# Kernel tuning notes

Hardware: AMD Instinct MI355X
Metric: run time of the kernel (lower is better)

## Reference

```python
import jax, jax.numpy as jnp
import numpy as np

NUM_EMBEDDINGS = 1024
EMBEDDING_DIM = 128
COMMITMENT_COST = 1.0
DECAY = 0.99
EPSILON = 1e-05
N_TOKENS = 65536


def setup_inputs() -> dict:
    key = jax.random.key(0)
    k1, k2, k3 = jax.random.split(key, 3)
    inputs = jax.random.normal(k1, (N_TOKENS, EMBEDDING_DIM), dtype=jnp.float32)
    embedding = jax.random.normal(k2, (NUM_EMBEDDINGS, EMBEDDING_DIM), dtype=jnp.float32) * 0.01
    cluster_size = jnp.ones((NUM_EMBEDDINGS,), dtype=jnp.float32)
    embed_avg = jax.random.normal(k3, (NUM_EMBEDDINGS, EMBEDDING_DIM), dtype=jnp.float32) * 0.01
    return {"inputs": inputs, "embedding": embedding,
            "cluster_size": cluster_size, "embed_avg": embed_avg}


def reference(inputs, embedding, cluster_size, embed_avg):
    # inputs: [N, D], embedding: [K, D]
    flat = inputs.reshape(-1, EMBEDDING_DIM)
    distances = (jnp.sum(flat * flat, axis=1, keepdims=True)
                 + jnp.sum(embedding * embedding, axis=1)
                 - 2.0 * flat @ embedding.T)
    idx = jnp.argmin(distances, axis=1)                       # [N]
    quantized = embedding[idx].reshape(inputs.shape)          # direct gather (same math as one-hot matmul)

    # EMA update (training path); one-hot matmuls replaced by bincount/segment_sum
    dw = jnp.zeros((NUM_EMBEDDINGS,), dtype=flat.dtype).at[idx].add(1.0)   # encodings.sum(0)
    new_cluster_size = cluster_size * DECAY + (1.0 - DECAY) * dw
    dw_embed = jax.ops.segment_sum(flat, idx, num_segments=NUM_EMBEDDINGS)  # encodings.T @ flat
    new_embed_avg = embed_avg * DECAY + (1.0 - DECAY) * dw_embed
    n = jnp.sum(new_cluster_size)
    cs = (new_cluster_size + EPSILON) / (n + NUM_EMBEDDINGS * EPSILON) * n
    new_embedding = new_embed_avg / cs[:, None]

    # losses (quantized/inputs detach semantics are identical values in fwd)
    diff2 = jnp.mean((quantized - inputs) ** 2)
    loss = diff2 + COMMITMENT_COST * diff2

    # straight-through estimator: value equals quantized
    quantized_st = inputs + jax.lax.stop_gradient(quantized - inputs)
    return (quantized_st, loss, idx, new_embedding, new_cluster_size, new_embed_avg)
```

## Files before the change

### kernel.cpp

```cpp
#include <hip/hip_runtime.h>

typedef __attribute__((ext_vector_type(8))) _Float16 half8;
typedef __attribute__((ext_vector_type(4))) float f32x4;

constexpr int NTOK = 65536;
constexpr int DIM  = 128;
constexpr int NK   = 1024;

__global__ void bprep_k(const float* __restrict__ emb, char* __restrict__ bp,
                        float* __restrict__ embT, float* __restrict__ e2s,
                        double* __restrict__ en2d, int* __restrict__ nflag) {
  int i = blockIdx.x * 256 + threadIdx.x;
  if (i == 0) *nflag = 0;
  int c = i >> 4;
  int g = i & 15;
  float4 v0 = *(const float4*)&emb[c * 128 + g * 8];
  float4 v1 = *(const float4*)&emb[c * 128 + g * 8 + 4];
  float vf[8] = {v0.x, v0.y, v0.z, v0.w, v1.x, v1.y, v1.z, v1.w};
  half8 hv;
  double pacc = 0.0;
#pragma unroll
  for (int j = 0; j < 8; j++) {
    hv[j] = (_Float16)vf[j];
    embT[(g * 8 + j) * NK + c] = vf[j];
    pacc = fma((double)vf[j], (double)vf[j], pacc);
  }
  int chunk = c >> 5, n = (c >> 4) & 1, cl = c & 15;
  int kk = g >> 2, lo4 = g & 3;
  *(half8*)(bp + chunk * 8192 + kk * 2048 + n * 1024 + (lo4 * 16 + cl) * 16) = hv;
#pragma unroll
  for (int mask = 1; mask < 16; mask <<= 1) pacc += __shfl_xor(pacc, mask);
  if (g == 0) {
    en2d[c] = pacc;
    e2s[c] = (float)(pacc * 134217728.0 + 1073741824.0);
  }
}

__global__ __launch_bounds__(128, 2)
void argmin_k(const float* __restrict__ x, const char* __restrict__ bp,
              const float* __restrict__ e2s, int* __restrict__ idx_arr,
              float* __restrict__ out_idx, int* __restrict__ nflag,
              int* __restrict__ flags) {
  __shared__ unsigned kvs[2][32], k2s[2][32];
  const int t    = threadIdx.x;
  const int lane = t & 63;
  const int w    = t >> 6;
  const int l15  = lane & 15;
  const int lo4  = lane >> 4;
  const int rbase = blockIdx.x * 32;
  const int cbase = w * 16;
  const int lb16 = lane * 16;

  half8 FA[4][2], FB[4][2];

#define LOADG(DST, C, KK)                                                      \
  {                                                                            \
    const char* _b = bp + ((C) * 8192 + (KK) * 2048) + lb16;                   \
    DST[0] = *(const half8*)_b;                                                \
    DST[1] = *(const half8*)(_b + 1024);                                       \
  }

#pragma unroll
  for (int kk = 0; kk < 4; kk++) LOADG(FA[kk], cbase, kk)
#pragma unroll
  for (int kk = 0; kk < 4; kk++) LOADG(FB[kk], cbase + 1, kk)

  half8 ah[2][4];
#pragma unroll
  for (int m = 0; m < 2; m++)
#pragma unroll
    for (int kk = 0; kk < 4; kk++) {
      const float* xp = &x[(rbase + m * 16 + l15) * 128 + kk * 32 + lo4 * 8];
      float4 v0 = *(const float4*)xp;
      float4 v1 = *(const float4*)(xp + 4);
      float vf[8] = {v0.x, v0.y, v0.z, v0.w, v1.x, v1.y, v1.z, v1.w};
      half8 av;
#pragma unroll
      for (int j = 0; j < 8; j++) av[j] = (_Float16)vf[j];
      ah[m][kk] = av;
    }

  unsigned bv[2][4], b2[2][4];
#pragma unroll
  for (int m = 0; m < 2; m++)
#pragma unroll
    for (int r = 0; r < 4; r++) { bv[m][r] = 0xFFFFFFFFu; b2[m][r] = 0xFFFFFFFFu; }

#define MFMA_PHASE(BANK, KK)                                                   \
  {                                                                            \
    acc[0][0] = __builtin_amdgcn_mfma_f32_16x16x32_f16(ah[0][KK], BANK[KK][0], acc[0][0], 0, 0, 0); \
    acc[1][0] = __builtin_amdgcn_mfma_f32_16x16x32_f16(ah[1][KK], BANK[KK][0], acc[1][0], 0, 0, 0); \
    acc[0][1] = __builtin_amdgcn_mfma_f32_16x16x32_f16(ah[0][KK], BANK[KK][1], acc[0][1], 0, 0, 0); \
    acc[1][1] = __builtin_amdgcn_mfma_f32_16x16x32_f16(ah[1][KK], BANK[KK][1], acc[1][1], 0, 0, 0); \
  }

#define KEY_EPI(C)                                                             \
  {                                                                            \
    _Pragma("unroll")                                                          \
    for (int n = 0; n < 2; n++) {                                              \
      unsigned col = (unsigned)((C) * 32 + n * 16 + l15);                      \
      float e2v = n ? e2b : e2a;                                               \
      _Pragma("unroll")                                                        \
      for (int m = 0; m < 2; m++)                                              \
        _Pragma("unroll")                                                      \
        for (int r = 0; r < 4; r++) {                                          \
          float ks = fmaf(acc[m][n][r], -268435456.0f, e2v);                   \
          unsigned key = ((unsigned)ks & 0xFFFFFC00u) | col;                   \
          unsigned old = bv[m][r];                                             \
          bv[m][r] = min(old, key);                                            \
          b2[m][r] = min(b2[m][r], max(old, key));                             \
        }                                                                      \
    }                                                                          \
  }

  for (int i = 0; i < 16; i += 2) {
    const int cg = cbase + i;
    {
      float e2a = e2s[cg * 32 + l15];
      float e2b = e2s[cg * 32 + 16 + l15];
      f32x4 acc[2][2];
#pragma unroll
      for (int m = 0; m < 2; m++)
#pragma unroll
        for (int n = 0; n < 2; n++) acc[m][n] = (f32x4)(0.0f);
#pragma unroll
      for (int kk = 0; kk < 4; kk++) {
        MFMA_PHASE(FA, kk)
        if (i + 2 < 16) LOADG(FA[kk], cg + 2, kk)
      }
      KEY_EPI(cg)
    }
    {
      float e2a = e2s[(cg + 1) * 32 + l15];
      float e2b = e2s[(cg + 1) * 32 + 16 + l15];
      f32x4 acc[2][2];
#pragma unroll
      for (int m = 0; m < 2; m++)
#pragma unroll
        for (int n = 0; n < 2; n++) acc[m][n] = (f32x4)(0.0f);
#pragma unroll
      for (int kk = 0; kk < 4; kk++) {
        MFMA_PHASE(FB, kk)
        if (i + 3 < 16) LOADG(FB[kk], cg + 3, kk)
      }
      KEY_EPI(cg + 1)
    }
  }
#undef LOADG
#undef MFMA_PHASE
#undef KEY_EPI

#pragma unroll
  for (int m = 0; m < 2; m++)
#pragma unroll
    for (int r = 0; r < 4; r++) {
      unsigned v = bv[m][r], v2 = b2[m][r];
      for (int mask = 1; mask < 16; mask <<= 1) {
        unsigned ov = __shfl_xor(v, mask);
        unsigned o2 = __shfl_xor(v2, mask);
        v2 = min(min(v2, o2), max(v, ov));
        v  = min(v, ov);
      }
      if (l15 == 0) {
        int lr = m * 16 + lo4 * 4 + r;
        kvs[w][lr] = v;
        k2s[w][lr] = v2;
      }
    }
  __syncthreads();

  if (t < 32) {
    unsigned va = kvs[0][t], vb = kvs[1][t];
    unsigned v2 = min(min(k2s[0][t], k2s[1][t]), max(va, vb));
    unsigned v  = min(va, vb);
    int row = rbase + t;
    int ii = (int)(v & 1023u);
    idx_arr[row] = ii;
    out_idx[row] = (float)ii;
    if ((v2 >> 10) - (v >> 10) < 79u) {
      int p = atomicAdd(nflag, 1); flags[p] = row;
    }
  }
}

__global__ __launch_bounds__(256)
void fb_k(const float* __restrict__ x, const float* __restrict__ embT,
          const double* __restrict__ en2d, const int* __restrict__ nflag,
          const int* __restrict__ flags, int* __restrict__ idx_arr,
          float* __restrict__ out_idx) {
  int n = *nflag;
  __shared__ double xsh[4][DIM];
  __shared__ double sv[256];
  __shared__ int    si[256];
  int t = threadIdx.x;
  double n0 = en2d[t * 4 + 0], n1 = en2d[t * 4 + 1];
  double n2 = en2d[t * 4 + 2], n3 = en2d[t * 4 + 3];
  for (int base = blockIdx.x * 4; base < n; base += gridDim.x * 4) {
    int nb = min(4, n - base);
    __syncthreads();
    for (int u = t; u < nb * DIM; u += 256) {
      int j = u >> 7, d = u & 127;
      xsh[j][d] = (double)x[flags[base + j] * DIM + d];
    }
    __syncthreads();
    double xe[4][4];
#pragma unroll
    for (int j = 0; j < 4; j++)
#pragma unroll
      for (int q = 0; q < 4; q++) xe[j][q] = 0.0;
    for (int d = 0; d < DIM; d++) {
      float4 v = *(const float4*)&embT[d * NK + t * 4];
      double e0 = (double)v.x, e1 = (double)v.y, e2 = (double)v.z, e3 = (double)v.w;
#pragma unroll
      for (int j = 0; j < 4; j++) {
        double xd = xsh[j][d];
        xe[j][0] = fma(e0, xd, xe[j][0]);
        xe[j][1] = fma(e1, xd, xe[j][1]);
        xe[j][2] = fma(e2, xd, xe[j][2]);
        xe[j][3] = fma(e3, xd, xe[j][3]);
      }
    }
#pragma unroll
    for (int j = 0; j < 4; j++) {
      double s0 = n0 - 2.0 * xe[j][0];
      double s1 = n1 - 2.0 * xe[j][1];
      double s2 = n2 - 2.0 * xe[j][2];
      double s3 = n3 - 2.0 * xe[j][3];
      double bvv = s0; int bii = t * 4;
      if (s1 < bvv) { bvv = s1; bii = t * 4 + 1; }
      if (s2 < bvv) { bvv = s2; bii = t * 4 + 2; }
      if (s3 < bvv) { bvv = s3; bii = t * 4 + 3; }
      sv[t] = bvv; si[t] = bii;
      __syncthreads();
      for (int sh = 128; sh > 0; sh >>= 1) {
        if (t < sh) {
          double ov = sv[t + sh]; int oi = si[t + sh];
          if (ov < sv[t] || (ov == sv[t] && oi < si[t])) { sv[t] = ov; si[t] = oi; }
        }
        __syncthreads();
      }
      if (t == 0 && j < nb) {
        int row = flags[base + j];
        idx_arr[row] = si[0];
        out_idx[row] = (float)si[0];
      }
      __syncthreads();
    }
  }
}

__global__ void histb_k(const int* __restrict__ idx, unsigned* __restrict__ bcount) {
  __shared__ unsigned bins[NK];
  int t = threadIdx.x;
  for (int b = t; b < NK; b += 256) bins[b] = 0u;
  __syncthreads();
#pragma unroll
  for (int j = 0; j < 4; j++)
    atomicAdd(&bins[idx[blockIdx.x * 1024 + j * 256 + t]], 1u);
  __syncthreads();
  for (int b = t; b < NK; b += 256) bcount[blockIdx.x * NK + b] = bins[b];
}

__global__ void scan_k(unsigned* __restrict__ bcount, unsigned* __restrict__ icounts,
                       unsigned* __restrict__ offsets, const float* __restrict__ cs,
                       float* __restrict__ out_ncs, float* __restrict__ csk) {
  __shared__ unsigned sc[NK];
  __shared__ float sf[NK];
  int t = threadIdx.x;
  unsigned tot = 0;
#pragma unroll 8
  for (int b = 0; b < 64; b++) tot += bcount[b * NK + t];
  icounts[t] = tot;
  sc[t] = tot;
  __syncthreads();
  for (int off = 1; off < NK; off <<= 1) {
    unsigned v = (t >= off) ? sc[t - off] : 0u;
    __syncthreads();
    sc[t] += v;
    __syncthreads();
  }
  unsigned excl = sc[t] - tot;
  offsets[t] = excl;
  unsigned run = excl;
#pragma unroll 8
  for (int b = 0; b < 64; b++) {
    unsigned c = bcount[b * NK + t];
    bcount[b * NK + t] = run;
    run += c;
  }
  float c0 = cs[t];
  float ncs = c0 * 0.99f + 0.01f * (float)tot;
  out_ncs[t] = ncs;
  sf[t] = c0;
  __syncthreads();
  for (int s = 512; s > 0; s >>= 1) {
    if (t < s) sf[t] += sf[t + s];
    __syncthreads();
  }
  float n = 0.99f * sf[0] + 655.36f;
  csk[t] = (ncs + 1e-5f) / (n + 1024.0f * 1e-5f) * n;
}

__global__ __launch_bounds__(1024)
void scatter_k(const int* __restrict__ idx, const unsigned* __restrict__ bstart,
               int* __restrict__ order) {
  __shared__ unsigned cur[NK];
  int t = threadIdx.x;
  cur[t] = bstart[blockIdx.x * NK + t];
  __syncthreads();
  int r = blockIdx.x * 1024 + t;
  unsigned p = atomicAdd(&cur[idx[r]], 1u);
  order[p] = r;
}

__global__ __launch_bounds__(512)
void fgather_k(const float* __restrict__ x, const float* __restrict__ emb,
               const unsigned* __restrict__ offsets, const unsigned* __restrict__ icounts,
               const int* __restrict__ order, float* __restrict__ out_q,
               float* __restrict__ dwsum2, float* __restrict__ partial2) {
  __shared__ int ids[1024];
  int k = blockIdx.x >> 1, half = blockIdx.x & 1;
  int t = threadIdx.x;
  int d = t & 127, h = t >> 7;
  unsigned cnt = icounts[k];
  unsigned chl = cnt >> 1;
  unsigned s = offsets[k] + (half ? chl : 0u);
  unsigned myc = half ? (cnt - chl) : chl;
  for (unsigned j = t; j < myc && j < 1024u; j += 512) ids[j] = order[s + j];
  __syncthreads();
  float e = emb[k * DIM + d];
  float acc = 0.f, ls = 0.f;
#pragma unroll 4
  for (unsigned j = h; j < myc; j += 4) {
    int row = (j < 1024u) ? ids[j] : order[s + j];
    float xv = x[row * DIM + d];
    out_q[row * DIM + d] = e;
    acc += xv;
    float dd = e - xv;
    ls += dd * dd;
  }
  __shared__ float sa[512], sl[512];
  sa[t] = acc; sl[t] = ls;
  __syncthreads();
  if (t < 128) dwsum2[(half * NK + k) * DIM + t] = sa[t] + sa[t + 128] + sa[t + 256] + sa[t + 384];
  for (int sh = 256; sh > 0; sh >>= 1) {
    if (t < sh) sl[t] += sl[t + sh];
    __syncthreads();
  }
  if (t == 0) partial2[blockIdx.x] = sl[0];
}

__global__ void emb_k(const float* __restrict__ embed_avg, const float* __restrict__ dwsum2,
                      const float* __restrict__ csk, const float* __restrict__ partial2,
                      float* __restrict__ out_nemb, float* __restrict__ out_nea,
                      float* __restrict__ out_loss) {
  if (blockIdx.x == 0) {
    __shared__ float red[256];
    int t = threadIdx.x;
    float v = 0.f;
#pragma unroll
    for (int i = 0; i < 8; i++) v += partial2[t + 256 * i];
    red[t] = v;
    __syncthreads();
    for (int sh = 128; sh > 0; sh >>= 1) {
      if (t < sh) red[t] += red[t + sh];
      __syncthreads();
    }
    if (t == 0) out_loss[0] = 2.0f * red[0] / 8388608.0f;
    return;
  }
  int i = (blockIdx.x - 1) * 256 + threadIdx.x;
  float dw = dwsum2[i] + dwsum2[NK * DIM + i];
  float na = embed_avg[i] * 0.99f + 0.01f * dw;
  out_nea[i] = na;
  out_nemb[i] = na / csk[i >> 7];
}

extern "C" void kernel_launch(void* const* d_in, const int* in_sizes, int n_in,
                              void* d_out, int out_size, void* d_ws, size_t ws_size,
                              hipStream_t stream) {
  const float* x   = (const float*)d_in[0];
  const float* emb = (const float*)d_in[1];
  const float* cs  = (const float*)d_in[2];
  const float* ea  = (const float*)d_in[3];

  float* out      = (float*)d_out;
  float* out_q    = out;
  float* out_loss = out + 8388608;
  float* out_idx  = out + 8388609;
  float* out_nemb = out + 8454145;
  float* out_ncs  = out + 8585217;
  float* out_nea  = out + 8586241;

  float* W        = (float*)d_ws;
  float* e2s      = W;
  double* en2d    = (double*)(W + 1024);
  char*  bpack    = (char*)(W + 3072);
  float* embT     = W + 72704;
  unsigned* bcount = (unsigned*)(W + 203776);
  unsigned* icounts = (unsigned*)(W + 269312);
  unsigned* offsets = (unsigned*)(W + 270336);
  float* csk      = W + 271360;
  int*   nflag    = (int*)(W + 272384);
  int*   flags    = (int*)(W + 272400);
  int*   idx_arr  = (int*)(W + 337936);
  int*   order    = (int*)(W + 403472);
  float* dwsum2   = W + 469008;
  float* partial2 = W + 731152;

  bprep_k<<<64, 256, 0, stream>>>(emb, bpack, embT, e2s, en2d, nflag);
  argmin_k<<<2048, 128, 0, stream>>>(x, bpack, e2s, idx_arr, out_idx, nflag, flags);
  fb_k<<<256, 256, 0, stream>>>(x, embT, en2d, nflag, flags, idx_arr, out_idx);
  histb_k<<<64, 256, 0, stream>>>(idx_arr, bcount);
  scan_k<<<1, 1024, 0, stream>>>(bcount, icounts, offsets, cs, out_ncs, csk);
  scatter_k<<<64, 1024, 0, stream>>>(idx_arr, bcount, order);
  fgather_k<<<2048, 512, 0, stream>>>(x, emb, offsets, icounts, order, out_q, dwsum2, partial2);
  emb_k<<<513, 256, 0, stream>>>(ea, dwsum2, csk, partial2, out_nemb, out_nea, out_loss);
}
```

Before: 102.0 us.

## Double argmin row tile to 64 and split gather per code into four blocks

The argmin kernel now handles 64 rows per block instead of 32, so each loaded codebook B fragment feeds twice as many MFMAs and the grid halves. The gather/segment-sum kernel splits each code's rows across four blocks instead of two, which adds parallelism for unevenly sized clusters. The partial sums buffer grows to four slices, and emb_k reduces all four. The argmin change raises register pressure under the launch bounds and leaves fewer blocks to fill the device.

```diff
diff --git a/kernel.cpp b/kernel.cpp
--- a/kernel.cpp
+++ b/kernel.cpp
@@ -41,13 +41,13 @@
               const float* __restrict__ e2s, int* __restrict__ idx_arr,
               float* __restrict__ out_idx, int* __restrict__ nflag,
               int* __restrict__ flags) {
-  __shared__ unsigned kvs[2][32], k2s[2][32];
+  __shared__ unsigned kvs[2][64], k2s[2][64];
   const int t    = threadIdx.x;
   const int lane = t & 63;
   const int w    = t >> 6;
   const int l15  = lane & 15;
   const int lo4  = lane >> 4;
-  const int rbase = blockIdx.x * 32;
+  const int rbase = blockIdx.x * 64;
   const int cbase = w * 16;
   const int lb16 = lane * 16;
 
@@ -65,9 +65,9 @@
 #pragma unroll
   for (int kk = 0; kk < 4; kk++) LOADG(FB[kk], cbase + 1, kk)
 
-  half8 ah[2][4];
-#pragma unroll
-  for (int m = 0; m < 2; m++)
+  half8 ah[4][4];
+#pragma unroll
+  for (int m = 0; m < 4; m++)
 #pragma unroll
     for (int kk = 0; kk < 4; kk++) {
       const float* xp = &x[(rbase + m * 16 + l15) * 128 + kk * 32 + lo4 * 8];
@@ -80,18 +80,19 @@
       ah[m][kk] = av;
     }
 
-  unsigned bv[2][4], b2[2][4];
-#pragma unroll
-  for (int m = 0; m < 2; m++)
+  unsigned bv[4][4], b2[4][4];
+#pragma unroll
+  for (int m = 0; m < 4; m++)
 #pragma unroll
     for (int r = 0; r < 4; r++) { bv[m][r] = 0xFFFFFFFFu; b2[m][r] = 0xFFFFFFFFu; }
 
 #define MFMA_PHASE(BANK, KK)                                                   \
   {                                                                            \
-    acc[0][0] = __builtin_amdgcn_mfma_f32_16x16x32_f16(ah[0][KK], BANK[KK][0], acc[0][0], 0, 0, 0); \
-    acc[1][0] = __builtin_amdgcn_mfma_f32_16x16x32_f16(ah[1][KK], BANK[KK][0], acc[1][0], 0, 0, 0); \
-    acc[0][1] = __builtin_amdgcn_mfma_f32_16x16x32_f16(ah[0][KK], BANK[KK][1], acc[0][1], 0, 0, 0); \
-    acc[1][1] = __builtin_amdgcn_mfma_f32_16x16x32_f16(ah[1][KK], BANK[KK][1], acc[1][1], 0, 0, 0); \
+    _Pragma("unroll")                                                          \
+    for (int m = 0; m < 4; m++) {                                              \
+      acc[m][0] = __builtin_amdgcn_mfma_f32_16x16x32_f16(ah[m][KK], BANK[KK][0], acc[m][0], 0, 0, 0); \
+      acc[m][1] = __builtin_amdgcn_mfma_f32_16x16x32_f16(ah[m][KK], BANK[KK][1], acc[m][1], 0, 0, 0); \
+    }                                                                          \
   }
 
 #define KEY_EPI(C)                                                             \
@@ -101,7 +102,7 @@
       unsigned col = (unsigned)((C) * 32 + n * 16 + l15);                      \
       float e2v = n ? e2b : e2a;                                               \
       _Pragma("unroll")                                                        \
-      for (int m = 0; m < 2; m++)                                              \
+      for (int m = 0; m < 4; m++)                                              \
         _Pragma("unroll")                                                      \
         for (int r = 0; r < 4; r++) {                                          \
           float ks = fmaf(acc[m][n][r], -268435456.0f, e2v);                   \
@@ -118,9 +119,9 @@
     {
       float e2a = e2s[cg * 32 + l15];
       float e2b = e2s[cg * 32 + 16 + l15];
-      f32x4 acc[2][2];
-#pragma unroll
-      for (int m = 0; m < 2; m++)
+      f32x4 acc[4][2];
+#pragma unroll
+      for (int m = 0; m < 4; m++)
 #pragma unroll
         for (int n = 0; n < 2; n++) acc[m][n] = (f32x4)(0.0f);
 #pragma unroll
@@ -133,9 +134,9 @@
     {
       float e2a = e2s[(cg + 1) * 32 + l15];
       float e2b = e2s[(cg + 1) * 32 + 16 + l15];
-      f32x4 acc[2][2];
-#pragma unroll
-      for (int m = 0; m < 2; m++)
+      f32x4 acc[4][2];
+#pragma unroll
+      for (int m = 0; m < 4; m++)
 #pragma unroll
         for (int n = 0; n < 2; n++) acc[m][n] = (f32x4)(0.0f);
 #pragma unroll
@@ -151,7 +152,7 @@
 #undef KEY_EPI
 
 #pragma unroll
-  for (int m = 0; m < 2; m++)
+  for (int m = 0; m < 4; m++)
 #pragma unroll
     for (int r = 0; r < 4; r++) {
       unsigned v = bv[m][r], v2 = b2[m][r];
@@ -169,7 +170,7 @@
     }
   __syncthreads();
 
-  if (t < 32) {
+  if (t < 64) {
     unsigned va = kvs[0][t], vb = kvs[1][t];
     unsigned v2 = min(min(k2s[0][t], k2s[1][t]), max(va, vb));
     unsigned v  = min(va, vb);
@@ -317,20 +318,21 @@
 void fgather_k(const float* __restrict__ x, const float* __restrict__ emb,
                const unsigned* __restrict__ offsets, const unsigned* __restrict__ icounts,
                const int* __restrict__ order, float* __restrict__ out_q,
-               float* __restrict__ dwsum2, float* __restrict__ partial2) {
+               float* __restrict__ dwsum4, float* __restrict__ partial4) {
   __shared__ int ids[1024];
-  int k = blockIdx.x >> 1, half = blockIdx.x & 1;
+  int k = blockIdx.x >> 2, q = blockIdx.x & 3;
   int t = threadIdx.x;
   int d = t & 127, h = t >> 7;
   unsigned cnt = icounts[k];
-  unsigned chl = cnt >> 1;
-  unsigned s = offsets[k] + (half ? chl : 0u);
-  unsigned myc = half ? (cnt - chl) : chl;
+  unsigned qs = (cnt * (unsigned)q) >> 2;
+  unsigned qe = (cnt * (unsigned)(q + 1)) >> 2;
+  unsigned s = offsets[k] + qs;
+  unsigned myc = qe - qs;
   for (unsigned j = t; j < myc && j < 1024u; j += 512) ids[j] = order[s + j];
   __syncthreads();
   float e = emb[k * DIM + d];
   float acc = 0.f, ls = 0.f;
-#pragma unroll 4
+#pragma unroll 2
   for (unsigned j = h; j < myc; j += 4) {
     int row = (j < 1024u) ? ids[j] : order[s + j];
     float xv = x[row * DIM + d];
@@ -342,16 +344,16 @@
   __shared__ float sa[512], sl[512];
   sa[t] = acc; sl[t] = ls;
   __syncthreads();
-  if (t < 128) dwsum2[(half * NK + k) * DIM + t] = sa[t] + sa[t + 128] + sa[t + 256] + sa[t + 384];
+  if (t < 128) dwsum4[(q * NK + k) * DIM + t] = sa[t] + sa[t + 128] + sa[t + 256] + sa[t + 384];
   for (int sh = 256; sh > 0; sh >>= 1) {
     if (t < sh) sl[t] += sl[t + sh];
     __syncthreads();
   }
-  if (t == 0) partial2[blockIdx.x] = sl[0];
-}
-
-__global__ void emb_k(const float* __restrict__ embed_avg, const float* __restrict__ dwsum2,
-                      const float* __restrict__ csk, const float* __restrict__ partial2,
+  if (t == 0) partial4[blockIdx.x] = sl[0];
+}
+
+__global__ void emb_k(const float* __restrict__ embed_avg, const float* __restrict__ dwsum4,
+                      const float* __restrict__ csk, const float* __restrict__ partial4,
                       float* __restrict__ out_nemb, float* __restrict__ out_nea,
                       float* __restrict__ out_loss) {
   if (blockIdx.x == 0) {
@@ -359,7 +361,7 @@
     int t = threadIdx.x;
     float v = 0.f;
 #pragma unroll
-    for (int i = 0; i < 8; i++) v += partial2[t + 256 * i];
+    for (int i = 0; i < 16; i++) v += partial4[t + 256 * i];
     red[t] = v;
     __syncthreads();
     for (int sh = 128; sh > 0; sh >>= 1) {
@@ -370,7 +372,7 @@
     return;
   }
   int i = (blockIdx.x - 1) * 256 + threadIdx.x;
-  float dw = dwsum2[i] + dwsum2[NK * DIM + i];
+  float dw = dwsum4[i] + dwsum4[NK * DIM + i] + dwsum4[2 * NK * DIM + i] + dwsum4[3 * NK * DIM + i];
   float na = embed_avg[i] * 0.99f + 0.01f * dw;
   out_nea[i] = na;
   out_nemb[i] = na / csk[i >> 7];
@@ -405,15 +407,15 @@
   int*   flags    = (int*)(W + 272400);
   int*   idx_arr  = (int*)(W + 337936);
   int*   order    = (int*)(W + 403472);
-  float* dwsum2   = W + 469008;
-  float* partial2 = W + 731152;
+  float* dwsum4   = W + 469008;
+  float* partial4 = W + 993296;
 
   bprep_k<<<64, 256, 0, stream>>>(emb, bpack, embT, e2s, en2d, nflag);
-  argmin_k<<<2048, 128, 0, stream>>>(x, bpack, e2s, idx_arr, out_idx, nflag, flags);
+  argmin_k<<<1024, 128, 0, stream>>>(x, bpack, e2s, idx_arr, out_idx, nflag, flags);
   fb_k<<<256, 256, 0, stream>>>(x, embT, en2d, nflag, flags, idx_arr, out_idx);
   histb_k<<<64, 256, 0, stream>>>(idx_arr, bcount);
   scan_k<<<1, 1024, 0, stream>>>(bcount, icounts, offsets, cs, out_ncs, csk);
   scatter_k<<<64, 1024, 0, stream>>>(idx_arr, bcount, order);
-  fgather_k<<<2048, 512, 0, stream>>>(x, emb, offsets, icounts, order, out_q, dwsum2, partial2);
-  emb_k<<<513, 256, 0, stream>>>(ea, dwsum2, csk, partial2, out_nemb, out_nea, out_loss);
-}
+  fgather_k<<<4096, 512, 0, stream>>>(x, emb, offsets, icounts, order, out_q, dwsum4, partial4);
+  emb_k<<<513, 256, 0, stream>>>(ea, dwsum4, csk, partial4, out_nemb, out_nea, out_loss);
+}
```

Result: faster. 99.97 us (-2.0%).
